# Performance work log

Hardware: AMD Instinct MI355X
Metric: run time of the kernel (lower is better)

The kernel has to match this reference:

```python
import jax, jax.numpy as jnp
import numpy as np
from jax import lax

H = 128


def _lstm_dir(x, Wih, Whh, bih, bhh):
    # Single-direction LSTM, PyTorch gate order (i, f, g, o).
    # x: [B, L, D]; Wih: [4H, D]; Whh: [4H, H]; bih/bhh: [4H]
    B, L, _ = x.shape
    Hs = Whh.shape[1]
    # Precompute input contributions for all timesteps: [B, L, 4H]
    xg = jnp.einsum('bld,gd->blg', x, Wih) + bih + bhh

    def step(carry, g_t):
        h, c = carry
        g = g_t + h @ Whh.T
        i, f, gg, o = jnp.split(g, 4, axis=-1)
        c = jax.nn.sigmoid(f) * c + jax.nn.sigmoid(i) * jnp.tanh(gg)
        h = jax.nn.sigmoid(o) * jnp.tanh(c)
        return (h, c), h

    h0 = jnp.zeros((B, Hs), x.dtype)
    _, ys = lax.scan(step, (h0, h0), jnp.swapaxes(xg, 0, 1))  # [L, B, H]
    return jnp.swapaxes(ys, 0, 1)


def _bilstm(x, Wih, Whh, bih, bhh):
    # Wih: [2, 4H, D] (dir 0 = forward, dir 1 = backward)
    yf = _lstm_dir(x, Wih[0], Whh[0], bih[0], bhh[0])
    yb = _lstm_dir(x[:, ::-1], Wih[1], Whh[1], bih[1], bhh[1])[:, ::-1]
    return jnp.concatenate([yf, yb], axis=-1)


def _lstm_params(key, din):
    ks = jax.random.split(key, 4)
    s = 1.0 / np.sqrt(H)
    u = lambda k, shp: jax.random.uniform(k, shp, jnp.float32, -s, s)
    return (u(ks[0], (2, 4 * H, din)), u(ks[1], (2, 4 * H, H)),
            u(ks[2], (2, 4 * H)), u(ks[3], (2, 4 * H)))


def setup_inputs() -> dict:
    key = jax.random.key(0)
    ks = jax.random.split(key, 8)
    B, L, D, OUT = 128, 512, 13, 2
    inp = {'x': jax.random.normal(ks[0], (B, L, D), jnp.float32)}
    for name, din, k in [('1', D, ks[1]), ('21', 2 * H, ks[2]), ('22', D, ks[3]),
                         ('31', 4 * H, ks[4]), ('32', 2 * H, ks[5])]:
        Wih, Whh, bih, bhh = _lstm_params(k, din)
        inp['Wih' + name] = Wih
        inp['Whh' + name] = Whh
        inp['bih' + name] = bih
        inp['bhh' + name] = bhh
    s4 = 1.0 / np.sqrt(4 * H)
    sf = 1.0 / np.sqrt(H)
    k4 = jax.random.split(ks[6], 2)
    kf = jax.random.split(ks[7], 2)
    inp['l4_w'] = jax.random.uniform(k4[0], (H, 4 * H), jnp.float32, -s4, s4)
    inp['l4_b'] = jax.random.uniform(k4[1], (H,), jnp.float32, -s4, s4)
    inp['fc_w'] = jax.random.uniform(kf[0], (OUT, H), jnp.float32, -sf, sf)
    inp['fc_b'] = jax.random.uniform(kf[1], (OUT,), jnp.float32, -sf, sf)
    return inp


def reference(x, Wih1, Whh1, bih1, bhh1, Wih21, Whh21, bih21, bhh21,
              Wih22, Whh22, bih22, bhh22, Wih31, Whh31, bih31, bhh31,
              Wih32, Whh32, bih32, bhh32, l4_w, l4_b, fc_w, fc_b):
    y1 = _bilstm(x, Wih1, Whh1, bih1, bhh1)              # [B, L, 2H]
    y21 = _bilstm(y1, Wih21, Whh21, bih21, bhh21)        # [B, L, 2H]
    y22 = _bilstm(x, Wih22, Whh22, bih22, bhh22)         # [B, L, 2H]
    y2 = jnp.concatenate([y21, y22], axis=2)             # [B, L, 4H]
    y31 = _bilstm(y2, Wih31, Whh31, bih31, bhh31)        # [B, L, 2H]
    y32 = _bilstm(y21, Wih32, Whh32, bih32, bhh32)       # [B, L, 2H]
    y3 = jnp.max(jnp.concatenate([y31, y32], axis=2), axis=1)  # [B, 4H]
    y4 = jax.nn.selu(y3 @ l4_w.T + l4_b)                 # dropout is identity at eval
    return jax.nn.sigmoid(y4 @ fc_w.T + fc_b)            # [B, 2]
```

## Files before the change

### kernel.cpp

```cpp
#include <hip/hip_runtime.h>
#include <hip/hip_bf16.h>

typedef __attribute__((ext_vector_type(8))) short bf16x8;
typedef __attribute__((ext_vector_type(4))) float f32x4;
typedef __attribute__((ext_vector_type(2))) _Float16 f16x2;

__device__ __forceinline__ float bfbits(unsigned short u) {
  return __uint_as_float(((unsigned int)u) << 16);
}
__device__ __forceinline__ float sigf(float x) { return 1.f / (1.f + __expf(-x)); }
__device__ __forceinline__ float tanhf_(float x) {
  x = fminf(15.f, fmaxf(-15.f, x));
  float t = __expf(2.f * x);
  return (t - 1.f) / (t + 1.f);
}
#if __has_builtin(__builtin_amdgcn_fdot2)
__device__ __forceinline__ float FDOT2(f16x2 a, f16x2 b, float c) {
  return __builtin_amdgcn_fdot2(a, b, c, false);
}
#else
__device__ __forceinline__ float FDOT2(f16x2 a, f16x2 b, float c) {
  return c + (float)a.x * (float)b.x + (float)a.y * (float)b.y;
}
#endif
__device__ __forceinline__ f16x2 h2bc(unsigned int u) {
  return __builtin_bit_cast(f16x2, u);
}
__device__ __forceinline__ unsigned packh(float a, float b) {
  _Float16 ha = (_Float16)a, hb = (_Float16)b;
  return (unsigned)__builtin_bit_cast(unsigned short, ha) |
         ((unsigned)__builtin_bit_cast(unsigned short, hb) << 16);
}

__global__ __launch_bounds__(256) void wconv(
    const float* whh0, const float* whh1, const float* whh2, const float* whh3, const float* whh4,
    const float* wi21, const float* wi31, const float* wi32,
    const float* bi0, const float* bh0, const float* bi1, const float* bh1,
    const float* bi2, const float* bh2, const float* bi3, const float* bh3,
    const float* bi4, const float* bh4,
    float* whht, __hip_bfloat16* wihbf, float* bsum)
{
  int tid = blockIdx.x * 256 + threadIdx.x;
  if (tid < 5 * 131072) {
    int lay = tid / 131072, r = tid % 131072;
    const float* src = lay == 0 ? whh0 : lay == 1 ? whh1 : lay == 2 ? whh2 : lay == 3 ? whh3 : whh4;
    int d = r >> 16;
    int k = (r >> 9) & 127;
    int j = r & 511;
    whht[tid] = src[((size_t)d * 512 + j) * 128 + k];
    return;
  }
  int t2 = tid - 5 * 131072;
  if (t2 < 1048576) {
    const float* src; int idx;
    if (t2 < 262144)      { src = wi21; idx = t2; }
    else if (t2 < 786432) { src = wi31; idx = t2 - 262144; }
    else                  { src = wi32; idx = t2 - 786432; }
    wihbf[t2] = __float2bfloat16(src[idx]);
    return;
  }
  int t3 = t2 - 1048576;
  if (t3 < 5120) {
    int lay = t3 >> 10, idx = t3 & 1023;
    const float* bi = lay == 0 ? bi0 : lay == 1 ? bi1 : lay == 2 ? bi2 : lay == 3 ? bi3 : bi4;
    const float* bh = lay == 0 ? bh0 : lay == 1 ? bh1 : lay == 2 ? bh2 : lay == 3 ? bh3 : bh4;
    bsum[t3] = bi[idx] + bh[idx];
  }
}

__global__ __launch_bounds__(256) void projM(
    const __hip_bfloat16* __restrict__ A, int lda, int K,
    const __hip_bfloat16* __restrict__ Bw,
    const float* __restrict__ bsum,
    __hip_bfloat16* __restrict__ out)
{
  int d = blockIdx.z;
  const __hip_bfloat16* Bp = Bw + (size_t)d * 512 * K;
  const float* bs = bsum + d * 512;
  __hip_bfloat16* op = out + (size_t)d * 65536 * 512;
  int m0 = blockIdx.y * 128, n0 = blockIdx.x * 128;
  __shared__ __align__(16) __hip_bfloat16 As[128][32];
  __shared__ __align__(16) __hip_bfloat16 Bs[128][32];
  int tid = threadIdx.x, w = tid >> 6, l = tid & 63;
  int wm = (w >> 1) * 64, wn = (w & 1) * 64;
  f32x4 acc[4][4];
#pragma unroll
  for (int mi = 0; mi < 4; ++mi)
#pragma unroll
    for (int ni = 0; ni < 4; ++ni) acc[mi][ni] = (f32x4){0.f, 0.f, 0.f, 0.f};
  int srow = tid >> 2, sc = tid & 3;
  for (int k0 = 0; k0 < K; k0 += 32) {
#pragma unroll
    for (int p = 0; p < 2; ++p) {
      int row = p * 64 + srow;
      int slot = sc ^ (row & 3);
      uint4 va = *(const uint4*)(A + (size_t)(m0 + row) * lda + k0 + sc * 8);
      *(uint4*)(&As[row][slot * 8]) = va;
      uint4 vb = *(const uint4*)(Bp + (size_t)(n0 + row) * K + k0 + sc * 8);
      *(uint4*)(&Bs[row][slot * 8]) = vb;
    }
    __syncthreads();
    bf16x8 af[4], bfr[4];
#pragma unroll
    for (int mi = 0; mi < 4; ++mi) {
      int row = wm + mi * 16 + (l & 15);
      int slot = (l >> 4) ^ (row & 3);
      af[mi] = *(const bf16x8*)(&As[row][slot * 8]);
    }
#pragma unroll
    for (int ni = 0; ni < 4; ++ni) {
      int row = wn + ni * 16 + (l & 15);
      int slot = (l >> 4) ^ (row & 3);
      bfr[ni] = *(const bf16x8*)(&Bs[row][slot * 8]);
    }
#pragma unroll
    for (int mi = 0; mi < 4; ++mi)
#pragma unroll
      for (int ni = 0; ni < 4; ++ni)
        acc[mi][ni] = __builtin_amdgcn_mfma_f32_16x16x32_bf16(af[mi], bfr[ni], acc[mi][ni], 0, 0, 0);
    __syncthreads();
  }
#pragma unroll
  for (int ni = 0; ni < 4; ++ni) {
    int col = n0 + wn + ni * 16 + (l & 15);
    float bsv = bs[col];
#pragma unroll
    for (int mi = 0; mi < 4; ++mi) {
#pragma unroll
      for (int q = 0; q < 4; ++q) {
        int row = m0 + wm + mi * 16 + (l >> 4) * 4 + q;
        op[(size_t)row * 512 + col] = __float2bfloat16(acc[mi][ni][q] + bsv);
      }
    }
  }
}

struct ScanP {
  const __hip_bfloat16* xg;
  const float* wihx;
  const float* bs;
  const float* whht;
  __hip_bfloat16* yout; int ycols; int ycoloff;
  float* y3out; int y3off;
};

#define DOT32(W, HL, curx, S0, S1) { \
  const uint4* hb4_ = (const uint4*)&HL[curx][kq * 16]; \
  uint4 hA_ = hb4_[0], hB_ = hb4_[1]; \
  float a00_ = 0.f, a01_ = 0.f, a10_ = 0.f, a11_ = 0.f; \
  unsigned int u0_[8] = {hA_.x, hA_.y, hA_.z, hA_.w, hB_.x, hB_.y, hB_.z, hB_.w}; \
  _Pragma("unroll") \
  for (int m = 0; m < 8; m += 2) { \
    f16x2 h0_ = h2bc(u0_[m]), h1_ = h2bc(u0_[m + 1]); \
    a00_ = FDOT2(W[m], h0_, a00_);           a01_ = FDOT2(W[m + 1], h1_, a01_); \
    a10_ = FDOT2(W[16 + m], h0_, a10_);      a11_ = FDOT2(W[16 + m + 1], h1_, a11_); } \
  uint4 hC_ = hb4_[2], hD_ = hb4_[3]; \
  unsigned int u1_[8] = {hC_.x, hC_.y, hC_.z, hC_.w, hD_.x, hD_.y, hD_.z, hD_.w}; \
  _Pragma("unroll") \
  for (int m = 0; m < 8; m += 2) { \
    f16x2 h0_ = h2bc(u1_[m]), h1_ = h2bc(u1_[m + 1]); \
    a00_ = FDOT2(W[8 + m], h0_, a00_);       a01_ = FDOT2(W[8 + m + 1], h1_, a01_); \
    a10_ = FDOT2(W[24 + m], h0_, a10_);      a11_ = FDOT2(W[24 + m + 1], h1_, a11_); } \
  S0 = a00_ + a01_; S1 = a10_ + a11_; }

#define CELLPHASE(P, CT, PL, HL, CURX, TROW) { \
  int ct_ = (CT); \
  float gi = PL[0][ct_] + PL[1][ct_] + PL[2][ct_] + PL[3][ct_]; \
  float gf = PL[0][ct_ + 128] + PL[1][ct_ + 128] + PL[2][ct_ + 128] + PL[3][ct_ + 128]; \
  float gg = PL[0][ct_ + 256] + PL[1][ct_ + 256] + PL[2][ct_ + 256] + PL[3][ct_ + 256]; \
  float go = PL[0][ct_ + 384] + PL[1][ct_ + 384] + PL[2][ct_ + 384] + PL[3][ct_ + 384]; \
  creg = sigf(gf) * creg + sigf(gi) * tanhf_(gg); \
  float h_ = sigf(go) * tanhf_(creg); \
  _Float16 hf_ = (_Float16)h_; \
  ((unsigned short*)&HL[CURX][0])[ct_] = __builtin_bit_cast(unsigned short, hf_); \
  if (P.yout) P.yout[((size_t)b * 512 + (TROW)) * P.ycols + P.ycoloff + d * 128 + ct_] = __float2bfloat16(h_); \
  else mreg = fmaxf(mreg, h_); }

template<bool DUALB, bool FUSE>
__global__ __launch_bounds__(1024, 4) void scan7(ScanP pa, ScanP pb, const float* xin)
{
  const int b = blockIdx.x, d = blockIdx.y;
  const int tid = threadIdx.x;
  const int kq = tid >> 8, j2 = tid & 255;
  __shared__ unsigned int hA[2][64];
  __shared__ unsigned int hB[DUALB ? 2 : 1][64];
  __shared__ float pA[4][512];
  __shared__ float pB[DUALB ? 4 : 1][512];
  __shared__ unsigned int x_lds[FUSE ? 4096 : 4];

  f16x2 w16A[32], w16B[DUALB ? 32 : 1];
  {
    const float* wp = pa.whht + (size_t)d * 65536;
#pragma unroll
    for (int g2 = 0; g2 < 2; ++g2)
#pragma unroll
      for (int m = 0; m < 16; ++m) {
        int k = kq * 32 + 2 * m;
        int col = j2 + g2 * 256;
        f16x2 t;
        t.x = (_Float16)wp[(size_t)k * 512 + col];
        t.y = (_Float16)wp[(size_t)(k + 1) * 512 + col];
        w16A[g2 * 16 + m] = t;
      }
  }
  if (DUALB) {
    const float* wp = pb.whht + (size_t)d * 65536;
#pragma unroll
    for (int g2 = 0; g2 < 2; ++g2)
#pragma unroll
      for (int m = 0; m < 16; ++m) {
        int k = kq * 32 + 2 * m;
        int col = j2 + g2 * 256;
        f16x2 t;
        t.x = (_Float16)wp[(size_t)k * 512 + col];
        t.y = (_Float16)wp[(size_t)(k + 1) * 512 + col];
        w16B[g2 * 16 + m] = t;
      }
  }
#pragma unroll
  for (int i = 0; i < 32; ++i) asm volatile("" : "+v"(w16A[i]));
  if (DUALB) {
#pragma unroll
    for (int i = 0; i < 32; ++i) asm volatile("" : "+v"(w16B[i]));
  }

  f16x2 wxA[4], wxB[4];
  if (FUSE) {
    int kd = kq * 4;
#pragma unroll
    for (int g2 = 0; g2 < 2; ++g2) {
      int col = j2 + g2 * 256;
#pragma unroll
      for (int p = 0; p < 2; ++p) {
        int d0 = kd + 2 * p, d1 = kd + 2 * p + 1;
        float a0 = d0 < 13 ? pa.wihx[((size_t)d * 512 + col) * 13 + d0] : (d0 == 15 ? pa.bs[d * 512 + col] : 0.f);
        float a1 = d1 < 13 ? pa.wihx[((size_t)d * 512 + col) * 13 + d1] : (d1 == 15 ? pa.bs[d * 512 + col] : 0.f);
        f16x2 ta; ta.x = (_Float16)a0; ta.y = (_Float16)a1;
        wxA[g2 * 2 + p] = ta;
        float b0 = d0 < 13 ? pb.wihx[((size_t)d * 512 + col) * 13 + d0] : (d0 == 15 ? pb.bs[d * 512 + col] : 0.f);
        float b1 = d1 < 13 ? pb.wihx[((size_t)d * 512 + col) * 13 + d1] : (d1 == 15 ? pb.bs[d * 512 + col] : 0.f);
        f16x2 tb; tb.x = (_Float16)b0; tb.y = (_Float16)b1;
        wxB[g2 * 2 + p] = tb;
      }
    }
#pragma unroll
    for (int i = 0; i < 4; ++i) { asm volatile("" : "+v"(wxA[i])); asm volatile("" : "+v"(wxB[i])); }
    for (int i = tid; i < 4096; i += 1024) {
      int t_ = i >> 3, k_ = i & 7;
      int d0 = 2 * k_, d1 = 2 * k_ + 1;
      float v0 = d0 < 13 ? xin[((size_t)b * 512 + t_) * 13 + d0] : (d0 == 15 ? 1.f : 0.f);
      float v1 = d1 < 13 ? xin[((size_t)b * 512 + t_) * 13 + d1] : (d1 == 15 ? 1.f : 0.f);
      x_lds[i] = packh(v0, v1);
    }
  }

  const unsigned short* xga = FUSE ? (const unsigned short*)0
                                   : (const unsigned short*)pa.xg + ((size_t)(d * 128 + b)) * 262144;
  const unsigned short* xgb = (DUALB && !FUSE) ? (const unsigned short*)pb.xg + ((size_t)(d * 128 + b)) * 262144
                                               : (const unsigned short*)0;

  if (tid < 64) { hA[0][tid] = 0u; if (DUALB) hB[0][tid] = 0u; }
  float creg = 0.f, mreg = -1e30f;
  int curA = 0, curB = 0;
  int tt0 = d ? 511 : 0;
  unsigned short pfa0 = 0, pfa1 = 0, pfb0 = 0, pfb1 = 0;
  if (!FUSE && kq == 0) {
    pfa0 = xga[(size_t)tt0 * 512 + j2];
    pfa1 = xga[(size_t)tt0 * 512 + j2 + 256];
    if (DUALB) {
      pfb0 = xgb[(size_t)tt0 * 512 + j2];
      pfb1 = xgb[(size_t)tt0 * 512 + j2 + 256];
    }
  }
  __syncthreads();

  for (int t = 0; t < 512; ++t) {
    int tt = d ? 511 - t : t;
    int tn = (t + 1 < 512) ? t + 1 : 511;
    int ttn = d ? 511 - tn : tn;

    unsigned short pna0 = 0, pna1 = 0;
    if (!FUSE && kq == 0) {
      pna0 = xga[(size_t)ttn * 512 + j2];
      pna1 = xga[(size_t)ttn * 512 + j2 + 256];
    }
    {
      float s0, s1;
      DOT32(w16A, hA, curA, s0, s1);
      if (FUSE) {
        uint2 xv = *(const uint2*)&x_lds[tt * 8 + kq * 2];
        f16x2 x0 = h2bc(xv.x), x1 = h2bc(xv.y);
        s0 = FDOT2(wxA[0], x0, s0); s0 = FDOT2(wxA[1], x1, s0);
        s1 = FDOT2(wxA[2], x0, s1); s1 = FDOT2(wxA[3], x1, s1);
      } else if (kq == 0) {
        s0 += bfbits(pfa0); s1 += bfbits(pfa1);
      }
      pA[kq][j2] = s0;
      pA[kq][j2 + 256] = s1;
    }
    if (DUALB && t > 0 && tid >= 128 && tid < 256) {
      int ttpB = d ? 512 - t : t - 1;
      CELLPHASE(pb, tid - 128, pB, hB, curB ^ 1, ttpB);
    }
    __syncthreads();
    if (DUALB && t > 0) curB ^= 1;

    unsigned short pnb0 = 0, pnb1 = 0;
    if (DUALB) {
      if (!FUSE && kq == 0) {
        pnb0 = xgb[(size_t)ttn * 512 + j2];
        pnb1 = xgb[(size_t)ttn * 512 + j2 + 256];
      }
      float s0, s1;
      DOT32(w16B, hB, curB, s0, s1);
      if (FUSE) {
        uint2 xv = *(const uint2*)&x_lds[tt * 8 + kq * 2];
        f16x2 x0 = h2bc(xv.x), x1 = h2bc(xv.y);
        s0 = FDOT2(wxB[0], x0, s0); s0 = FDOT2(wxB[1], x1, s0);
        s1 = FDOT2(wxB[2], x0, s1); s1 = FDOT2(wxB[3], x1, s1);
      } else if (kq == 0) {
        s0 += bfbits(pfb0); s1 += bfbits(pfb1);
      }
      pB[kq][j2] = s0;
      pB[kq][j2 + 256] = s1;
    }
    if (tid < 128) {
      CELLPHASE(pa, tid, pA, hA, curA ^ 1, tt);
    }
    __syncthreads();
    curA ^= 1;
    pfa0 = pna0; pfa1 = pna1; pfb0 = pnb0; pfb1 = pnb1;
  }
  if (DUALB && tid >= 128 && tid < 256) {
    int ttpB = d ? 0 : 511;
    CELLPHASE(pb, tid - 128, pB, hB, curB ^ 1, ttpB);
  }
  if (!pa.yout && tid < 128)
    pa.y3out[(size_t)b * 512 + pa.y3off + d * 128 + tid] = mreg;
  if (DUALB && !pb.yout && tid >= 128 && tid < 256)
    pb.y3out[(size_t)b * 512 + pb.y3off + d * 128 + (tid - 128)] = mreg;
}

__global__ __launch_bounds__(256) void head(
    const float* __restrict__ y3, const float* __restrict__ l4w,
    const float* __restrict__ l4b, const float* __restrict__ fcw,
    const float* __restrict__ fcb, float* __restrict__ outp)
{
  int b = blockIdx.x, t = threadIdx.x;
  __shared__ float row[512];
  __shared__ float y4[128];
  row[t] = y3[(size_t)b * 512 + t];
  row[t + 256] = y3[(size_t)b * 512 + t + 256];
  __syncthreads();
  if (t < 128) {
    float acc = l4b[t];
    const float* wr = l4w + (size_t)t * 512;
    for (int k = 0; k < 512; ++k) acc += row[k] * wr[k];
    const float scale = 1.0507009873554804934193349852946f;
    const float alpha = 1.6732632423543772848170429916717f;
    y4[t] = acc > 0.f ? scale * acc : scale * alpha * (__expf(acc) - 1.f);
  }
  __syncthreads();
  if (t < 2) {
    float acc = fcb[t];
    const float* wr = fcw + (size_t)t * 128;
    for (int k = 0; k < 128; ++k) acc += y4[k] * wr[k];
    outp[b * 2 + t] = 1.f / (1.f + __expf(-acc));
  }
}

extern "C" void kernel_launch(void* const* d_in, const int* in_sizes, int n_in,
                              void* d_out, int out_size, void* d_ws, size_t ws_size,
                              hipStream_t stream) {
  (void)in_sizes; (void)n_in; (void)out_size;
  const float* x     = (const float*)d_in[0];
  const float* Wih1  = (const float*)d_in[1];
  const float* Whh1  = (const float*)d_in[2];
  const float* bih1  = (const float*)d_in[3];
  const float* bhh1  = (const float*)d_in[4];
  const float* Wih21 = (const float*)d_in[5];
  const float* Whh21 = (const float*)d_in[6];
  const float* bih21 = (const float*)d_in[7];
  const float* bhh21 = (const float*)d_in[8];
  const float* Wih22 = (const float*)d_in[9];
  const float* Whh22 = (const float*)d_in[10];
  const float* bih22 = (const float*)d_in[11];
  const float* bhh22 = (const float*)d_in[12];
  const float* Wih31 = (const float*)d_in[13];
  const float* Whh31 = (const float*)d_in[14];
  const float* bih31 = (const float*)d_in[15];
  const float* bhh31 = (const float*)d_in[16];
  const float* Wih32 = (const float*)d_in[17];
  const float* Whh32 = (const float*)d_in[18];
  const float* bih32 = (const float*)d_in[19];
  const float* bhh32 = (const float*)d_in[20];
  const float* l4w   = (const float*)d_in[21];
  const float* l4b   = (const float*)d_in[22];
  const float* fcw   = (const float*)d_in[23];
  const float* fcb   = (const float*)d_in[24];

  char* ws = (char*)d_ws;
  const size_t NEED_F31 = 340545536ull;
  bool f31 = (ws_size >= NEED_F31);

  __hip_bfloat16 *xgA, *xgB, *y1, *y2, *wihbf;
  float *y3, *bsum, *whht;
  if (f31) {
    xgA   = (__hip_bfloat16*)(ws);
    xgB   = (__hip_bfloat16*)(ws + 134217728);
    y1    = (__hip_bfloat16*)(ws + 134217728);
    y2    = (__hip_bfloat16*)(ws + 268435456);
    y3    = (float*)(ws + 335544320);
    wihbf = (__hip_bfloat16*)(ws + 335806464);
    bsum  = (float*)(ws + 337903616);
    whht  = (float*)(ws + 337924096);
  } else {
    xgA   = (__hip_bfloat16*)(ws);
    xgB   = xgA;
    y1    = (__hip_bfloat16*)(ws + 134217728);
    y2    = (__hip_bfloat16*)(ws + 167772160);
    y3    = (float*)(ws + 234881024);
    wihbf = (__hip_bfloat16*)(ws + 235143168);
    bsum  = (float*)(ws + 237240320);
    whht  = (float*)(ws + 237260800);
  }

  wconv<<<6676, 256, 0, stream>>>(Whh1, Whh21, Whh22, Whh31, Whh32,
                                  Wih21, Wih31, Wih32,
                                  bih1, bhh1, bih21, bhh21, bih22, bhh22,
                                  bih31, bhh31, bih32, bhh32,
                                  whht, wihbf, bsum);

  ScanP P1  = {nullptr, Wih1,  bsum + 0 * 1024, whht + 0 * 131072, y1, 256, 0,   nullptr, 0};
  ScanP P22 = {nullptr, Wih22, bsum + 2 * 1024, whht + 2 * 131072, y2, 512, 256, nullptr, 0};
  ScanP P21 = {xgA, nullptr, nullptr, whht + 1 * 131072, y2, 512, 0, nullptr, 0};
  ScanP P31 = {xgA, nullptr, nullptr, whht + 3 * 131072, nullptr, 0, 0, y3, 0};
  ScanP P32 = {xgB, nullptr, nullptr, whht + 4 * 131072, nullptr, 0, 0, y3, 256};

  scan7<true, true><<<dim3(128, 2), 1024, 0, stream>>>(P1, P22, x);
  projM<<<dim3(4, 512, 2), 256, 0, stream>>>(y1, 256, 256, wihbf + 0, bsum + 1 * 1024, xgA);
  scan7<false, false><<<dim3(128, 2), 1024, 0, stream>>>(P21, P21, nullptr);
  if (f31) {
    projM<<<dim3(4, 512, 2), 256, 0, stream>>>(y2, 512, 512, wihbf + 262144, bsum + 3 * 1024, xgA);
    projM<<<dim3(4, 512, 2), 256, 0, stream>>>(y2, 512, 256, wihbf + 786432, bsum + 4 * 1024, xgB);
    scan7<true, false><<<dim3(128, 2), 1024, 0, stream>>>(P31, P32, nullptr);
  } else {
    projM<<<dim3(4, 512, 2), 256, 0, stream>>>(y2, 512, 512, wihbf + 262144, bsum + 3 * 1024, xgA);
    scan7<false, false><<<dim3(128, 2), 1024, 0, stream>>>(P31, P31, nullptr);
    projM<<<dim3(4, 512, 2), 256, 0, stream>>>(y2, 512, 256, wihbf + 786432, bsum + 4 * 1024, xgA);
    scan7<false, false><<<dim3(128, 2), 1024, 0, stream>>>(P32, P32, nullptr);
  }
  head<<<128, 256, 0, stream>>>(y3, l4w, l4b, fcw, fcb, (float*)d_out);
}
```

Measured before the change: 2.115 ms.

## Restructure LSTM scan so each 8-lane group computes all four gates of one cell

The recurrent scan kernel is reorganised so that each group of 8 lanes owns one hidden unit, holds its slice of the recurrent weights for all four gates, and reduces the partial dot products with DPP cross-lane adds. The cell update then happens redundantly in every lane instead of through shared-memory partial-sum buffers, which removes one of the two block barriers per timestep and the LDS partial-sum traffic. The hidden-state buffer is padded to avoid bank conflicts. In exchange every lane evaluates the transcendental gate math and issues four input-gate loads per step, and the dual-layer variant no longer overlaps the two layers' phases.

```diff
diff --git a/kernel.cpp b/kernel.cpp
--- a/kernel.cpp
+++ b/kernel.cpp
@@ -30,6 +30,20 @@
   _Float16 ha = (_Float16)a, hb = (_Float16)b;
   return (unsigned)__builtin_bit_cast(unsigned short, ha) |
          ((unsigned)__builtin_bit_cast(unsigned short, hb) << 16);
+}
+
+__device__ __forceinline__ float red8(float s) {
+#if __has_builtin(__builtin_amdgcn_update_dpp)
+  int r1 = __builtin_amdgcn_update_dpp(0, __builtin_bit_cast(int, s), 0xB1, 0xF, 0xF, true);
+  s += __builtin_bit_cast(float, r1);
+  int r2 = __builtin_amdgcn_update_dpp(0, __builtin_bit_cast(int, s), 0x4E, 0xF, 0xF, true);
+  s += __builtin_bit_cast(float, r2);
+  int r3 = __builtin_amdgcn_update_dpp(0, __builtin_bit_cast(int, s), 0x141, 0xF, 0xF, true);
+  s += __builtin_bit_cast(float, r3);
+#else
+  s += __shfl_xor(s, 1); s += __shfl_xor(s, 2); s += __shfl_xor(s, 4);
+#endif
+  return s;
 }
 
 __global__ __launch_bounds__(256) void wconv(
@@ -144,132 +158,92 @@
   float* y3out; int y3off;
 };
 
-#define DOT32(W, HL, curx, S0, S1) { \
-  const uint4* hb4_ = (const uint4*)&HL[curx][kq * 16]; \
-  uint4 hA_ = hb4_[0], hB_ = hb4_[1]; \
-  float a00_ = 0.f, a01_ = 0.f, a10_ = 0.f, a11_ = 0.f; \
-  unsigned int u0_[8] = {hA_.x, hA_.y, hA_.z, hA_.w, hB_.x, hB_.y, hB_.z, hB_.w}; \
-  _Pragma("unroll") \
-  for (int m = 0; m < 8; m += 2) { \
-    f16x2 h0_ = h2bc(u0_[m]), h1_ = h2bc(u0_[m + 1]); \
-    a00_ = FDOT2(W[m], h0_, a00_);           a01_ = FDOT2(W[m + 1], h1_, a01_); \
-    a10_ = FDOT2(W[16 + m], h0_, a10_);      a11_ = FDOT2(W[16 + m + 1], h1_, a11_); } \
-  uint4 hC_ = hb4_[2], hD_ = hb4_[3]; \
-  unsigned int u1_[8] = {hC_.x, hC_.y, hC_.z, hC_.w, hD_.x, hD_.y, hD_.z, hD_.w}; \
-  _Pragma("unroll") \
-  for (int m = 0; m < 8; m += 2) { \
-    f16x2 h0_ = h2bc(u1_[m]), h1_ = h2bc(u1_[m + 1]); \
-    a00_ = FDOT2(W[8 + m], h0_, a00_);       a01_ = FDOT2(W[8 + m + 1], h1_, a01_); \
-    a10_ = FDOT2(W[24 + m], h0_, a10_);      a11_ = FDOT2(W[24 + m + 1], h1_, a11_); } \
-  S0 = a00_ + a01_; S1 = a10_ + a11_; }
-
-#define CELLPHASE(P, CT, PL, HL, CURX, TROW) { \
-  int ct_ = (CT); \
-  float gi = PL[0][ct_] + PL[1][ct_] + PL[2][ct_] + PL[3][ct_]; \
-  float gf = PL[0][ct_ + 128] + PL[1][ct_ + 128] + PL[2][ct_ + 128] + PL[3][ct_ + 128]; \
-  float gg = PL[0][ct_ + 256] + PL[1][ct_ + 256] + PL[2][ct_ + 256] + PL[3][ct_ + 256]; \
-  float go = PL[0][ct_ + 384] + PL[1][ct_ + 384] + PL[2][ct_ + 384] + PL[3][ct_ + 384]; \
-  creg = sigf(gf) * creg + sigf(gi) * tanhf_(gg); \
-  float h_ = sigf(go) * tanhf_(creg); \
-  _Float16 hf_ = (_Float16)h_; \
-  ((unsigned short*)&HL[CURX][0])[ct_] = __builtin_bit_cast(unsigned short, hf_); \
-  if (P.yout) P.yout[((size_t)b * 512 + (TROW)) * P.ycols + P.ycoloff + d * 128 + ct_] = __float2bfloat16(h_); \
-  else mreg = fmaxf(mreg, h_); }
-
 template<bool DUALB, bool FUSE>
-__global__ __launch_bounds__(1024, 4) void scan7(ScanP pa, ScanP pb, const float* xin)
+__global__ __launch_bounds__(1024, 4) void scan8(ScanP pa, ScanP pb, const float* xin)
 {
   const int b = blockIdx.x, d = blockIdx.y;
   const int tid = threadIdx.x;
-  const int kq = tid >> 8, j2 = tid & 255;
-  __shared__ unsigned int hA[2][64];
-  __shared__ unsigned int hB[DUALB ? 2 : 1][64];
-  __shared__ float pA[4][512];
-  __shared__ float pB[DUALB ? 4 : 1][512];
+  const int c = tid >> 3, q = tid & 7;
+  __shared__ __align__(16) unsigned int hpA[2][96];
+  __shared__ __align__(16) unsigned int hpB[DUALB ? 2 : 1][96];
   __shared__ unsigned int x_lds[FUSE ? 4096 : 4];
 
-  f16x2 w16A[32], w16B[DUALB ? 32 : 1];
+  f16x2 wA[32], wB[DUALB ? 32 : 1];
   {
-    const float* wp = pa.whht + (size_t)d * 65536;
-#pragma unroll
-    for (int g2 = 0; g2 < 2; ++g2)
-#pragma unroll
-      for (int m = 0; m < 16; ++m) {
-        int k = kq * 32 + 2 * m;
-        int col = j2 + g2 * 256;
+    const float* wp = pa.whht + (size_t)d * 65536 + (size_t)(q * 16) * 512 + c;
+#pragma unroll
+    for (int g = 0; g < 4; ++g)
+#pragma unroll
+      for (int m = 0; m < 8; ++m) {
         f16x2 t;
-        t.x = (_Float16)wp[(size_t)k * 512 + col];
-        t.y = (_Float16)wp[(size_t)(k + 1) * 512 + col];
-        w16A[g2 * 16 + m] = t;
+        t.x = (_Float16)wp[(size_t)(2 * m) * 512 + g * 128];
+        t.y = (_Float16)wp[(size_t)(2 * m + 1) * 512 + g * 128];
+        wA[g * 8 + m] = t;
       }
   }
   if (DUALB) {
-    const float* wp = pb.whht + (size_t)d * 65536;
-#pragma unroll
-    for (int g2 = 0; g2 < 2; ++g2)
-#pragma unroll
-      for (int m = 0; m < 16; ++m) {
-        int k = kq * 32 + 2 * m;
-        int col = j2 + g2 * 256;
+    const float* wp = pb.whht + (size_t)d * 65536 + (size_t)(q * 16) * 512 + c;
+#pragma unroll
+    for (int g = 0; g < 4; ++g)
+#pragma unroll
+      for (int m = 0; m < 8; ++m) {
         f16x2 t;
-        t.x = (_Float16)wp[(size_t)k * 512 + col];
-        t.y = (_Float16)wp[(size_t)(k + 1) * 512 + col];
-        w16B[g2 * 16 + m] = t;
-      }
-  }
-#pragma unroll
-  for (int i = 0; i < 32; ++i) asm volatile("" : "+v"(w16A[i]));
+        t.x = (_Float16)wp[(size_t)(2 * m) * 512 + g * 128];
+        t.y = (_Float16)wp[(size_t)(2 * m + 1) * 512 + g * 128];
+        wB[g * 8 + m] = t;
+      }
+  }
+#pragma unroll
+  for (int i = 0; i < 32; ++i) asm volatile("" : "+v"(wA[i]));
   if (DUALB) {
 #pragma unroll
-    for (int i = 0; i < 32; ++i) asm volatile("" : "+v"(w16B[i]));
+    for (int i = 0; i < 32; ++i) asm volatile("" : "+v"(wB[i]));
   }
 
   f16x2 wxA[4], wxB[4];
   if (FUSE) {
-    int kd = kq * 4;
-#pragma unroll
-    for (int g2 = 0; g2 < 2; ++g2) {
-      int col = j2 + g2 * 256;
-#pragma unroll
-      for (int p = 0; p < 2; ++p) {
-        int d0 = kd + 2 * p, d1 = kd + 2 * p + 1;
-        float a0 = d0 < 13 ? pa.wihx[((size_t)d * 512 + col) * 13 + d0] : (d0 == 15 ? pa.bs[d * 512 + col] : 0.f);
-        float a1 = d1 < 13 ? pa.wihx[((size_t)d * 512 + col) * 13 + d1] : (d1 == 15 ? pa.bs[d * 512 + col] : 0.f);
-        f16x2 ta; ta.x = (_Float16)a0; ta.y = (_Float16)a1;
-        wxA[g2 * 2 + p] = ta;
-        float b0 = d0 < 13 ? pb.wihx[((size_t)d * 512 + col) * 13 + d0] : (d0 == 15 ? pb.bs[d * 512 + col] : 0.f);
-        float b1 = d1 < 13 ? pb.wihx[((size_t)d * 512 + col) * 13 + d1] : (d1 == 15 ? pb.bs[d * 512 + col] : 0.f);
-        f16x2 tb; tb.x = (_Float16)b0; tb.y = (_Float16)b1;
-        wxB[g2 * 2 + p] = tb;
-      }
-    }
-#pragma unroll
-    for (int i = 0; i < 4; ++i) { asm volatile("" : "+v"(wxA[i])); asm volatile("" : "+v"(wxB[i])); }
+    int d0 = 2 * q, d1 = 2 * q + 1;
+#pragma unroll
+    for (int g = 0; g < 4; ++g) {
+      int col = g * 128 + c;
+      float a0 = d0 < 13 ? pa.wihx[((size_t)d * 512 + col) * 13 + d0] : 0.f;
+      float a1 = d1 < 13 ? pa.wihx[((size_t)d * 512 + col) * 13 + d1]
+                         : (d1 == 15 ? pa.bs[d * 512 + col] : 0.f);
+      f16x2 ta; ta.x = (_Float16)a0; ta.y = (_Float16)a1;
+      wxA[g] = ta;
+      float b0 = d0 < 13 ? pb.wihx[((size_t)d * 512 + col) * 13 + d0] : 0.f;
+      float b1 = d1 < 13 ? pb.wihx[((size_t)d * 512 + col) * 13 + d1]
+                         : (d1 == 15 ? pb.bs[d * 512 + col] : 0.f);
+      f16x2 tb; tb.x = (_Float16)b0; tb.y = (_Float16)b1;
+      wxB[g] = tb;
+    }
     for (int i = tid; i < 4096; i += 1024) {
       int t_ = i >> 3, k_ = i & 7;
-      int d0 = 2 * k_, d1 = 2 * k_ + 1;
-      float v0 = d0 < 13 ? xin[((size_t)b * 512 + t_) * 13 + d0] : (d0 == 15 ? 1.f : 0.f);
-      float v1 = d1 < 13 ? xin[((size_t)b * 512 + t_) * 13 + d1] : (d1 == 15 ? 1.f : 0.f);
+      int e0 = 2 * k_, e1 = 2 * k_ + 1;
+      float v0 = e0 < 13 ? xin[((size_t)b * 512 + t_) * 13 + e0] : 0.f;
+      float v1 = e1 < 13 ? xin[((size_t)b * 512 + t_) * 13 + e1] : (e1 == 15 ? 1.f : 0.f);
       x_lds[i] = packh(v0, v1);
     }
   }
 
   const unsigned short* xga = FUSE ? (const unsigned short*)0
                                    : (const unsigned short*)pa.xg + ((size_t)(d * 128 + b)) * 262144;
-  const unsigned short* xgb = (DUALB && !FUSE) ? (const unsigned short*)pb.xg + ((size_t)(d * 128 + b)) * 262144
-                                               : (const unsigned short*)0;
-
-  if (tid < 64) { hA[0][tid] = 0u; if (DUALB) hB[0][tid] = 0u; }
-  float creg = 0.f, mreg = -1e30f;
-  int curA = 0, curB = 0;
+  const unsigned short* xgb = (DUALB && !FUSE)
+                                   ? (const unsigned short*)pb.xg + ((size_t)(d * 128 + b)) * 262144
+                                   : (const unsigned short*)0;
+
+  if (tid < 96) { hpA[0][tid] = 0u; if (DUALB) hpB[0][tid] = 0u; }
+  float cA = 0.f, cB = 0.f, mA = -1e30f, mB = -1e30f;
+  int cur = 0;
   int tt0 = d ? 511 : 0;
-  unsigned short pfa0 = 0, pfa1 = 0, pfb0 = 0, pfb1 = 0;
-  if (!FUSE && kq == 0) {
-    pfa0 = xga[(size_t)tt0 * 512 + j2];
-    pfa1 = xga[(size_t)tt0 * 512 + j2 + 256];
-    if (DUALB) {
-      pfb0 = xgb[(size_t)tt0 * 512 + j2];
-      pfb1 = xgb[(size_t)tt0 * 512 + j2 + 256];
+  unsigned short pfA[4], pfB[4];
+#pragma unroll
+  for (int g = 0; g < 4; ++g) { pfA[g] = 0; pfB[g] = 0; }
+  if (!FUSE) {
+#pragma unroll
+    for (int g = 0; g < 4; ++g) {
+      pfA[g] = xga[(size_t)tt0 * 512 + g * 128 + c];
+      if (DUALB) pfB[g] = xgb[(size_t)tt0 * 512 + g * 128 + c];
     }
   }
   __syncthreads();
@@ -278,67 +252,94 @@
     int tt = d ? 511 - t : t;
     int tn = (t + 1 < 512) ? t + 1 : 511;
     int ttn = d ? 511 - tn : tn;
-
-    unsigned short pna0 = 0, pna1 = 0;
-    if (!FUSE && kq == 0) {
-      pna0 = xga[(size_t)ttn * 512 + j2];
-      pna1 = xga[(size_t)ttn * 512 + j2 + 256];
-    }
+    unsigned short pnA[4], pnB[4];
+#pragma unroll
+    for (int g = 0; g < 4; ++g) { pnA[g] = 0; pnB[g] = 0; }
+    if (!FUSE) {
+#pragma unroll
+      for (int g = 0; g < 4; ++g) {
+        pnA[g] = xga[(size_t)ttn * 512 + g * 128 + c];
+        if (DUALB) pnB[g] = xgb[(size_t)ttn * 512 + g * 128 + c];
+      }
+    }
+
     {
-      float s0, s1;
-      DOT32(w16A, hA, curA, s0, s1);
+      const uint4* hb = (const uint4*)&hpA[cur][q * 12];
+      uint4 h0 = hb[0], h1 = hb[1];
+      unsigned hu[8] = {h0.x, h0.y, h0.z, h0.w, h1.x, h1.y, h1.z, h1.w};
+      float s0 = 0.f, s1 = 0.f, s2 = 0.f, s3 = 0.f;
+#pragma unroll
+      for (int m = 0; m < 8; ++m) {
+        f16x2 hh = h2bc(hu[m]);
+        s0 = FDOT2(wA[m], hh, s0);
+        s1 = FDOT2(wA[8 + m], hh, s1);
+        s2 = FDOT2(wA[16 + m], hh, s2);
+        s3 = FDOT2(wA[24 + m], hh, s3);
+      }
       if (FUSE) {
-        uint2 xv = *(const uint2*)&x_lds[tt * 8 + kq * 2];
-        f16x2 x0 = h2bc(xv.x), x1 = h2bc(xv.y);
-        s0 = FDOT2(wxA[0], x0, s0); s0 = FDOT2(wxA[1], x1, s0);
-        s1 = FDOT2(wxA[2], x0, s1); s1 = FDOT2(wxA[3], x1, s1);
-      } else if (kq == 0) {
-        s0 += bfbits(pfa0); s1 += bfbits(pfa1);
-      }
-      pA[kq][j2] = s0;
-      pA[kq][j2 + 256] = s1;
-    }
-    if (DUALB && t > 0 && tid >= 128 && tid < 256) {
-      int ttpB = d ? 512 - t : t - 1;
-      CELLPHASE(pb, tid - 128, pB, hB, curB ^ 1, ttpB);
+        f16x2 xv = h2bc(x_lds[tt * 8 + q]);
+        s0 = FDOT2(wxA[0], xv, s0); s1 = FDOT2(wxA[1], xv, s1);
+        s2 = FDOT2(wxA[2], xv, s2); s3 = FDOT2(wxA[3], xv, s3);
+      }
+      s0 = red8(s0); s1 = red8(s1); s2 = red8(s2); s3 = red8(s3);
+      if (!FUSE) {
+        s0 += bfbits(pfA[0]); s1 += bfbits(pfA[1]);
+        s2 += bfbits(pfA[2]); s3 += bfbits(pfA[3]);
+      }
+      cA = sigf(s1) * cA + sigf(s0) * tanhf_(s2);
+      float h = sigf(s3) * tanhf_(cA);
+      if (q == 0) {
+        _Float16 hf = (_Float16)h;
+        ((unsigned short*)&hpA[cur ^ 1][0])[(c >> 4) * 24 + (c & 15)] =
+            __builtin_bit_cast(unsigned short, hf);
+        if (pa.yout)
+          pa.yout[((size_t)b * 512 + tt) * pa.ycols + pa.ycoloff + d * 128 + c] = __float2bfloat16(h);
+      }
+      if (!pa.yout) mA = fmaxf(mA, h);
+    }
+    if (DUALB) {
+      const uint4* hb = (const uint4*)&hpB[cur][q * 12];
+      uint4 h0 = hb[0], h1 = hb[1];
+      unsigned hu[8] = {h0.x, h0.y, h0.z, h0.w, h1.x, h1.y, h1.z, h1.w};
+      float s0 = 0.f, s1 = 0.f, s2 = 0.f, s3 = 0.f;
+#pragma unroll
+      for (int m = 0; m < 8; ++m) {
+        f16x2 hh = h2bc(hu[m]);
+        s0 = FDOT2(wB[m], hh, s0);
+        s1 = FDOT2(wB[8 + m], hh, s1);
+        s2 = FDOT2(wB[16 + m], hh, s2);
+        s3 = FDOT2(wB[24 + m], hh, s3);
+      }
+      if (FUSE) {
+        f16x2 xv = h2bc(x_lds[tt * 8 + q]);
+        s0 = FDOT2(wxB[0], xv, s0); s1 = FDOT2(wxB[1], xv, s1);
+        s2 = FDOT2(wxB[2], xv, s2); s3 = FDOT2(wxB[3], xv, s3);
+      }
+      s0 = red8(s0); s1 = red8(s1); s2 = red8(s2); s3 = red8(s3);
+      if (!FUSE) {
+        s0 += bfbits(pfB[0]); s1 += bfbits(pfB[1]);
+        s2 += bfbits(pfB[2]); s3 += bfbits(pfB[3]);
+      }
+      cB = sigf(s1) * cB + sigf(s0) * tanhf_(s2);
+      float h = sigf(s3) * tanhf_(cB);
+      if (q == 0) {
+        _Float16 hf = (_Float16)h;
+        ((unsigned short*)&hpB[cur ^ 1][0])[(c >> 4) * 24 + (c & 15)] =
+            __builtin_bit_cast(unsigned short, hf);
+        if (pb.yout)
+          pb.yout[((size_t)b * 512 + tt) * pb.ycols + pb.ycoloff + d * 128 + c] = __float2bfloat16(h);
+      }
+      if (!pb.yout) mB = fmaxf(mB, h);
     }
     __syncthreads();
-    if (DUALB && t > 0) curB ^= 1;
-
-    unsigned short pnb0 = 0, pnb1 = 0;
-    if (DUALB) {
-      if (!FUSE && kq == 0) {
-        pnb0 = xgb[(size_t)ttn * 512 + j2];
-        pnb1 = xgb[(size_t)ttn * 512 + j2 + 256];
-      }
-      float s0, s1;
-      DOT32(w16B, hB, curB, s0, s1);
-      if (FUSE) {
-        uint2 xv = *(const uint2*)&x_lds[tt * 8 + kq * 2];
-        f16x2 x0 = h2bc(xv.x), x1 = h2bc(xv.y);
-        s0 = FDOT2(wxB[0], x0, s0); s0 = FDOT2(wxB[1], x1, s0);
-        s1 = FDOT2(wxB[2], x0, s1); s1 = FDOT2(wxB[3], x1, s1);
-      } else if (kq == 0) {
-        s0 += bfbits(pfb0); s1 += bfbits(pfb1);
-      }
-      pB[kq][j2] = s0;
-      pB[kq][j2 + 256] = s1;
-    }
-    if (tid < 128) {
-      CELLPHASE(pa, tid, pA, hA, curA ^ 1, tt);
-    }
-    __syncthreads();
-    curA ^= 1;
-    pfa0 = pna0; pfa1 = pna1; pfb0 = pnb0; pfb1 = pnb1;
-  }
-  if (DUALB && tid >= 128 && tid < 256) {
-    int ttpB = d ? 0 : 511;
-    CELLPHASE(pb, tid - 128, pB, hB, curB ^ 1, ttpB);
-  }
-  if (!pa.yout && tid < 128)
-    pa.y3out[(size_t)b * 512 + pa.y3off + d * 128 + tid] = mreg;
-  if (DUALB && !pb.yout && tid >= 128 && tid < 256)
-    pb.y3out[(size_t)b * 512 + pb.y3off + d * 128 + (tid - 128)] = mreg;
+    cur ^= 1;
+#pragma unroll
+    for (int g = 0; g < 4; ++g) { pfA[g] = pnA[g]; pfB[g] = pnB[g]; }
+  }
+  if (!pa.yout && q == 0)
+    pa.y3out[(size_t)b * 512 + pa.y3off + d * 128 + c] = mA;
+  if (DUALB && !pb.yout && q == 0)
+    pb.y3out[(size_t)b * 512 + pb.y3off + d * 128 + c] = mB;
 }
 
 __global__ __launch_bounds__(256) void head(
@@ -437,18 +438,18 @@
   ScanP P31 = {xgA, nullptr, nullptr, whht + 3 * 131072, nullptr, 0, 0, y3, 0};
   ScanP P32 = {xgB, nullptr, nullptr, whht + 4 * 131072, nullptr, 0, 0, y3, 256};
 
-  scan7<true, true><<<dim3(128, 2), 1024, 0, stream>>>(P1, P22, x);
+  scan8<true, true><<<dim3(128, 2), 1024, 0, stream>>>(P1, P22, x);
   projM<<<dim3(4, 512, 2), 256, 0, stream>>>(y1, 256, 256, wihbf + 0, bsum + 1 * 1024, xgA);
-  scan7<false, false><<<dim3(128, 2), 1024, 0, stream>>>(P21, P21, nullptr);
+  scan8<false, false><<<dim3(128, 2), 1024, 0, stream>>>(P21, P21, nullptr);
   if (f31) {
     projM<<<dim3(4, 512, 2), 256, 0, stream>>>(y2, 512, 512, wihbf + 262144, bsum + 3 * 1024, xgA);
     projM<<<dim3(4, 512, 2), 256, 0, stream>>>(y2, 512, 256, wihbf + 786432, bsum + 4 * 1024, xgB);
-    scan7<true, false><<<dim3(128, 2), 1024, 0, stream>>>(P31, P32, nullptr);
+    scan8<true, false><<<dim3(128, 2), 1024, 0, stream>>>(P31, P32, nullptr);
   } else {
     projM<<<dim3(4, 512, 2), 256, 0, stream>>>(y2, 512, 512, wihbf + 262144, bsum + 3 * 1024, xgA);
-    scan7<false, false><<<dim3(128, 2), 1024, 0, stream>>>(P31, P31, nullptr);
+    scan8<false, false><<<dim3(128, 2), 1024, 0, stream>>>(P31, P31, nullptr);
     projM<<<dim3(4, 512, 2), 256, 0, stream>>>(y2, 512, 256, wihbf + 786432, bsum + 4 * 1024, xgA);
-    scan7<false, false><<<dim3(128, 2), 1024, 0, stream>>>(P32, P32, nullptr);
+    scan8<false, false><<<dim3(128, 2), 1024, 0, stream>>>(P32, P32, nullptr);
   }
   head<<<128, 256, 0, stream>>>(y3, l4w, l4b, fcw, fcb, (float*)d_out);
 }
```

Result: slower. 3.416 ms (+61.5%).
